# Kernel tuning notes

Measured on AMD Instinct MI355X. Metric: run time of the kernel, lower is better.

## Reference

```python
import jax, jax.numpy as jnp
import numpy as np
import math

D_MODEL = 1024
HEADS = 16
HEAD_DIM = D_MODEL // HEADS
FFN = 4096
B, S = 2, 2048


def _layer_norm(x, gamma, beta, eps=1e-5):
    mean = jnp.mean(x, axis=-1, keepdims=True)
    var = jnp.mean((x - mean) ** 2, axis=-1, keepdims=True)
    return gamma * (x - mean) / jnp.sqrt(var + eps) + beta


def _sdpa(q, k, v, mask):
    # q,k,v: [B,H,S,dh]; mask: [S,S] additive, broadcasts over B,H
    scaled = jnp.einsum('bhqd,bhkd->bhqk', q, k) / math.sqrt(q.shape[-1])
    scaled = scaled + mask
    attn = jax.nn.softmax(scaled, axis=-1)
    return jnp.einsum('bhqk,bhkd->bhqd', attn, v)


def setup_inputs() -> dict:
    key = jax.random.key(0)
    ks = jax.random.split(key, 12)
    s = 0.02
    inp = {
        'x': jax.random.normal(ks[0], (B, S, D_MODEL), jnp.float32),
        'y': jax.random.normal(ks[1], (B, S, D_MODEL), jnp.float32),
        'self_attention_mask': jnp.zeros((S, S), jnp.float32),
        'cross_attention_mask': jnp.zeros((S, S), jnp.float32),
        # self-attention params
        'Wqkv': jax.random.normal(ks[2], (D_MODEL, 3 * D_MODEL), jnp.float32) * s,
        'bqkv': jnp.zeros((3 * D_MODEL,), jnp.float32),
        'Wo1': jax.random.normal(ks[3], (D_MODEL, D_MODEL), jnp.float32) * s,
        'bo1': jnp.zeros((D_MODEL,), jnp.float32),
        # cross-attention params
        'Wkv': jax.random.normal(ks[4], (D_MODEL, 2 * D_MODEL), jnp.float32) * s,
        'bkv': jnp.zeros((2 * D_MODEL,), jnp.float32),
        'Wq': jax.random.normal(ks[5], (D_MODEL, D_MODEL), jnp.float32) * s,
        'bq': jnp.zeros((D_MODEL,), jnp.float32),
        'Wo2': jax.random.normal(ks[6], (D_MODEL, D_MODEL), jnp.float32) * s,
        'bo2': jnp.zeros((D_MODEL,), jnp.float32),
        # layer norms
        'g1': jnp.ones((D_MODEL,), jnp.float32), 'b1': jnp.zeros((D_MODEL,), jnp.float32),
        'g2': jnp.ones((D_MODEL,), jnp.float32), 'b2': jnp.zeros((D_MODEL,), jnp.float32),
        'g3': jnp.ones((D_MODEL,), jnp.float32), 'b3': jnp.zeros((D_MODEL,), jnp.float32),
        # FFN
        'W1': jax.random.normal(ks[7], (D_MODEL, FFN), jnp.float32) * s,
        'bw1': jnp.zeros((FFN,), jnp.float32),
        'W2': jax.random.normal(ks[8], (FFN, D_MODEL), jnp.float32) * s,
        'bw2': jnp.zeros((D_MODEL,), jnp.float32),
    }
    return inp


def reference(x, y, self_attention_mask, cross_attention_mask,
              Wqkv, bqkv, Wo1, bo1, Wkv, bkv, Wq, bq, Wo2, bo2,
              g1, b1, g2, b2, g3, b3, W1, bw1, W2, bw2):
    b, s, d = y.shape

    # ---- masked self-attention on y ----
    qkv = (y @ Wqkv + bqkv).reshape(b, s, HEADS, 3 * HEAD_DIM).transpose(0, 2, 1, 3)
    q, k, v = jnp.split(qkv, 3, axis=-1)  # each [B,H,S,dh]
    vals = _sdpa(q, k, v, self_attention_mask)
    vals = vals.transpose(0, 2, 1, 3).reshape(b, s, d)
    attn_out = vals @ Wo1 + bo1
    # dropout is identity at inference
    y1 = _layer_norm(attn_out + y, g1, b1)

    # ---- cross attention: q from y1, k/v from x ----
    kv = (x @ Wkv + bkv).reshape(b, s, HEADS, 2 * HEAD_DIM).transpose(0, 2, 1, 3)
    k2, v2 = jnp.split(kv, 2, axis=-1)
    q2 = (y1 @ Wq + bq).reshape(b, s, HEADS, HEAD_DIM).transpose(0, 2, 1, 3)
    vals2 = _sdpa(q2, k2, v2, cross_attention_mask)
    vals2 = vals2.transpose(0, 2, 1, 3).reshape(b, s, d)
    cross_out = vals2 @ Wo2 + bo2
    y2 = _layer_norm(cross_out + y1, g2, b2)

    # ---- FFN ----
    h = jax.nn.relu(y2 @ W1 + bw1)
    ffn_out = h @ W2 + bw2
    y3 = _layer_norm(ffn_out + y2, g3, b3)
    return y3
```

## Files before the change

### kernel.cpp

```cpp
#include <hip/hip_runtime.h>
#include <hip/hip_bf16.h>

#define SEQ      2048
#define BATCH    2
#define DMODEL   1024
#define NHEADS   16
#define HDIM     64
#define FFN_DIM  4096
#define MROWS    (BATCH*SEQ)

typedef __attribute__((ext_vector_type(8))) short bf16x8;
typedef __attribute__((ext_vector_type(4))) float f32x4;

__device__ __forceinline__ unsigned short f2b(float f) {
    union { float f; unsigned int u; } v; v.f = f;
    unsigned int u = v.u;
    return (unsigned short)((u + 0x7FFFu + ((u >> 16) & 1u)) >> 16);
}
__device__ __forceinline__ float b2f(unsigned short h) {
    union { unsigned int u; float f; } v; v.u = ((unsigned int)h) << 16;
    return v.f;
}
__device__ __forceinline__ void gload_lds16(const void* g, void* l) {
    __builtin_amdgcn_global_load_lds((const __attribute__((address_space(1))) void*)g,
                                     (__attribute__((address_space(3))) void*)l, 16, 0, 0);
}

__global__ __launch_bounds__(256) void wtrans(const float* __restrict__ W,
                                              unsigned short* __restrict__ Wt,
                                              int K, int N) {
    __shared__ float t[32][33];
    const int n0 = blockIdx.x * 32, k0 = blockIdx.y * 32;
    const int tx = threadIdx.x, ty = threadIdx.y;
#pragma unroll
    for (int i = 0; i < 4; i++)
        t[ty + i * 8][tx] = W[(size_t)(k0 + ty + i * 8) * N + n0 + tx];
    __syncthreads();
#pragma unroll
    for (int i = 0; i < 4; i++) {
        const int n = ty + i * 8;
        Wt[(size_t)(n0 + n) * K + k0 + tx] = f2b(t[tx][n]);
    }
}

__global__ __launch_bounds__(256) void tobf16(const float* __restrict__ in,
                                              unsigned short* __restrict__ out, int n) {
    const int i = (blockIdx.x * 256 + threadIdx.x) * 8;
    if (i >= n) return;
    float4 a = *(const float4*)(in + i);
    float4 b = *(const float4*)(in + i + 4);
    unsigned short r[8] = {f2b(a.x), f2b(a.y), f2b(a.z), f2b(a.w),
                           f2b(b.x), f2b(b.y), f2b(b.z), f2b(b.w)};
    *(uint4*)(out + i) = *(const uint4*)r;
}

template <int RELU, int WF32, int WB16>
__global__ __launch_bounds__(256) void gemm_bt(const unsigned short* __restrict__ A,
                                               const unsigned short* __restrict__ Bt,
                                               const float* __restrict__ bias,
                                               float* __restrict__ Cf,
                                               unsigned short* __restrict__ Cb,
                                               int M, int N, int K) {
    __shared__ __align__(16) unsigned short As[128 * 32];
    __shared__ __align__(16) unsigned short Bs[128 * 32];
    const int tid  = threadIdx.x;
    const int lane = tid & 63;
    const int w    = tid >> 6;
    const int m0   = blockIdx.y << 7;
    const int n0   = blockIdx.x << 7;
    const int wr   = (w >> 1) << 6;
    const int wc   = (w & 1) << 6;
    const int srow = lane >> 2;
    const int scol = (lane & 3) << 3;

    f32x4 acc[4][4];
#pragma unroll
    for (int mi = 0; mi < 4; mi++)
#pragma unroll
        for (int ni = 0; ni < 4; ni++) acc[mi][ni] = (f32x4){0.f, 0.f, 0.f, 0.f};

    for (int k0 = 0; k0 < K; k0 += 32) {
#pragma unroll
        for (int t = 0; t < 2; t++) {
            const int rg  = w * 2 + t;
            const int row = (rg << 4) + srow;
            gload_lds16(A  + (size_t)(m0 + row) * K + k0 + scol, (char*)As + (rg << 10));
            gload_lds16(Bt + (size_t)(n0 + row) * K + k0 + scol, (char*)Bs + (rg << 10));
        }
        __syncthreads();
        const int fr = lane & 15;
        const int fk = (lane >> 4) << 3;
        bf16x8 af[4], bfr[4];
#pragma unroll
        for (int i = 0; i < 4; i++) {
            af[i]  = *(const bf16x8*)(As + (wr + (i << 4) + fr) * 32 + fk);
            bfr[i] = *(const bf16x8*)(Bs + (wc + (i << 4) + fr) * 32 + fk);
        }
#pragma unroll
        for (int mi = 0; mi < 4; mi++)
#pragma unroll
            for (int ni = 0; ni < 4; ni++)
                acc[mi][ni] = __builtin_amdgcn_mfma_f32_16x16x32_bf16(af[mi], bfr[ni], acc[mi][ni], 0, 0, 0);
        __syncthreads();
    }

    const int fr = lane & 15;
    const int fq = lane >> 4;
#pragma unroll
    for (int mi = 0; mi < 4; mi++) {
#pragma unroll
        for (int ni = 0; ni < 4; ni++) {
            const int col = n0 + wc + (ni << 4) + fr;
            const float bv = bias[col];
#pragma unroll
            for (int i = 0; i < 4; i++) {
                const int row = m0 + wr + (mi << 4) + (fq << 2) + i;
                float v = acc[mi][ni][i] + bv;
                if (RELU) v = fmaxf(v, 0.f);
                if (WF32) Cf[(size_t)row * N + col] = v;
                if (WB16) Cb[(size_t)row * N + col] = f2b(v);
            }
        }
    }
}

template <int WB16>
__global__ __launch_bounds__(256) void resid_ln(const float* __restrict__ xin,
                                                const float* __restrict__ res,
                                                const float* __restrict__ g,
                                                const float* __restrict__ b,
                                                float* __restrict__ outf,
                                                unsigned short* __restrict__ outb) {
    const int row = blockIdx.x;
    const int tid = threadIdx.x;
    const size_t base = (size_t)row * 1024 + tid * 4;
    float4 xv = *(const float4*)(xin + base);
    float4 rv = *(const float4*)(res + base);
    const float v0 = xv.x + rv.x, v1 = xv.y + rv.y, v2 = xv.z + rv.z, v3 = xv.w + rv.w;
    float s  = v0 + v1 + v2 + v3;
    float sq = v0 * v0 + v1 * v1 + v2 * v2 + v3 * v3;
#pragma unroll
    for (int off = 32; off; off >>= 1) { s += __shfl_xor(s, off); sq += __shfl_xor(sq, off); }
    __shared__ float red[8];
    if ((tid & 63) == 0) { red[tid >> 6] = s; red[4 + (tid >> 6)] = sq; }
    __syncthreads();
    s  = red[0] + red[1] + red[2] + red[3];
    sq = red[4] + red[5] + red[6] + red[7];
    const float mean = s * (1.0f / 1024.0f);
    const float var  = sq * (1.0f / 1024.0f) - mean * mean;
    const float inv  = rsqrtf(var + 1e-5f);
    const int col = tid * 4;
    float4 gv = *(const float4*)(g + col);
    float4 bv = *(const float4*)(b + col);
    const float o0 = (v0 - mean) * inv * gv.x + bv.x;
    const float o1 = (v1 - mean) * inv * gv.y + bv.y;
    const float o2 = (v2 - mean) * inv * gv.z + bv.z;
    const float o3 = (v3 - mean) * inv * gv.w + bv.w;
    float4 ov = {o0, o1, o2, o3};
    *(float4*)(outf + base) = ov;
    if (WB16) {
        uint2 u;
        u.x = (unsigned int)f2b(o0) | ((unsigned int)f2b(o1) << 16);
        u.y = (unsigned int)f2b(o2) | ((unsigned int)f2b(o3) << 16);
        *(uint2*)(outb + base) = u;
    }
}

__global__ __launch_bounds__(256) void attn_mfma(
    const unsigned short* __restrict__ Qb, int q_rs, int q_ho,
    const unsigned short* __restrict__ Kb, int k_rs, int k_ho,
    const unsigned short* __restrict__ Vb, int v_rs, int v_ho,
    const float* __restrict__ mask,
    unsigned short* __restrict__ Ob, int o_rs, int o_ho) {
    __shared__ __align__(16) unsigned short Kls[64 * 64];
    __shared__ __align__(16) unsigned short Vraw[64 * 64];
    __shared__ __align__(16) unsigned short QVt[64 * 64];
    __shared__ __align__(16) unsigned short Pls[4][16 * 64];

    const int tid  = threadIdx.x;
    const int lane = tid & 63;
    const int w    = tid >> 6;
    const int g    = lane >> 4;
    const int q15  = lane & 15;
    const int swz  = (lane & 7) << 4;
    const int bh   = blockIdx.y;
    const int b    = bh >> 4, h = bh & 15;
    const int q0   = blockIdx.x << 6;
    const size_t rowbase = (size_t)b * SEQ;

    char* Kc = (char*)Kls;
    char* Vc = (char*)Vraw;
    char* Tc = (char*)QVt;
    char* Pc = (char*)(&Pls[w][0]);

    const int hq = h * q_ho, hk = h * k_ho, hv = h * v_ho;

    auto stage2 = [&](const unsigned short* base, int rs, int hoff, int row0, char* ldsb) {
#pragma unroll
        for (int bb = 0; bb < 2; bb++) {
            const int c = tid + (bb << 8);
            const int r = c >> 3, ci = c & 7;
            gload_lds16(base + (rowbase + row0 + r) * (size_t)rs + hoff + ((ci ^ (r & 7)) << 3),
                        ldsb + ((c >> 6) << 10));
        }
    };

    stage2(Qb, q_rs, hq, q0, Tc);
    stage2(Kb, k_rs, hk, 0, Kc);
    stage2(Vb, v_rs, hv, 0, Vc);

    float m_run = -3.0e38f, l_run = 0.f;
    f32x4 oacc[4];
#pragma unroll
    for (int fd = 0; fd < 4; fd++) oacc[fd] = (f32x4){0.f, 0.f, 0.f, 0.f};

    __syncthreads();
    bf16x8 qf[2];
#pragma unroll
    for (int s = 0; s < 2; s++)
        qf[s] = *(const bf16x8*)(Tc + (w * 16 + q15) * 128 + (((s << 6) + (g << 4)) ^ swz));
    __syncthreads();

    const float* mrow_ptr = mask + (size_t)(q0 + w * 16 + q15) * SEQ;

    for (int t = 0; t < 32; t++) {
        const int kv0 = t << 6;
#pragma unroll
        for (int bb = 0; bb < 2; bb++) {
            const int kvb = bb * 32 + w * 8;
            unsigned short t8[8];
#pragma unroll
            for (int m = 0; m < 8; m++)
                t8[m] = *(const unsigned short*)(Vc + (kvb + m) * 128 + ((2 * lane) ^ (m << 4)));
            *(uint4*)(Tc + lane * 128 + ((2 * kvb) ^ swz)) = *(const uint4*)t8;
        }
        f32x4 sacc[4];
#pragma unroll
        for (int f = 0; f < 4; f++) sacc[f] = (f32x4){0.f, 0.f, 0.f, 0.f};
#pragma unroll
        for (int s = 0; s < 2; s++)
#pragma unroll
            for (int f = 0; f < 4; f++) {
                bf16x8 kf = *(const bf16x8*)(Kc + (f * 16 + q15) * 128 + (((s << 6) + (g << 4)) ^ swz));
                sacc[f] = __builtin_amdgcn_mfma_f32_16x16x32_bf16(kf, qf[s], sacc[f], 0, 0, 0);
            }
        float p[4][4];
        float mt = -3.0e38f;
#pragma unroll
        for (int f = 0; f < 4; f++) {
            float4 mk = *(const float4*)(mrow_ptr + kv0 + f * 16 + g * 4);
            const float* mkp = (const float*)&mk;
#pragma unroll
            for (int r = 0; r < 4; r++) {
                const float v = sacc[f][r] * 0.125f + mkp[r];
                p[f][r] = v;
                mt = fmaxf(mt, v);
            }
        }
        mt = fmaxf(mt, __shfl_xor(mt, 16));
        mt = fmaxf(mt, __shfl_xor(mt, 32));
        const float mnew  = fmaxf(m_run, mt);
        const float alpha = __expf(m_run - mnew);
        m_run = mnew;
        float lsum = 0.f;
#pragma unroll
        for (int f = 0; f < 4; f++)
#pragma unroll
            for (int r = 0; r < 4; r++) {
                const float e = __expf(p[f][r] - mnew);
                p[f][r] = e;
                lsum += e;
            }
        lsum += __shfl_xor(lsum, 16);
        lsum += __shfl_xor(lsum, 32);
        l_run = l_run * alpha + lsum;
#pragma unroll
        for (int f = 0; f < 4; f++) {
            const unsigned int w0 = (unsigned int)f2b(p[f][0]) | ((unsigned int)f2b(p[f][1]) << 16);
            const unsigned int w1 = (unsigned int)f2b(p[f][2]) | ((unsigned int)f2b(p[f][3]) << 16);
            const int bbase = ((f << 5) + (g << 3)) ^ swz;
            *(unsigned int*)(Pc + q15 * 128 + bbase)     = w0;
            *(unsigned int*)(Pc + q15 * 128 + bbase + 4) = w1;
        }
        __syncthreads();
        if (t < 31) {
            stage2(Kb, k_rs, hk, kv0 + 64, Kc);
            stage2(Vb, v_rs, hv, kv0 + 64, Vc);
        }
        float ar[4];
#pragma unroll
        for (int r = 0; r < 4; r++) ar[r] = __shfl(alpha, (g << 4) + (g << 2) + r);
#pragma unroll
        for (int fd = 0; fd < 4; fd++)
#pragma unroll
            for (int r = 0; r < 4; r++) oacc[fd][r] *= ar[r];
#pragma unroll
        for (int s = 0; s < 2; s++) {
            const bf16x8 pf = *(const bf16x8*)(Pc + q15 * 128 + (((s << 6) + (g << 4)) ^ swz));
#pragma unroll
            for (int fd = 0; fd < 4; fd++) {
                const bf16x8 vf = *(const bf16x8*)(Tc + (fd * 16 + q15) * 128 + (((s << 6) + (g << 4)) ^ swz));
                oacc[fd] = __builtin_amdgcn_mfma_f32_16x16x32_bf16(pf, vf, oacc[fd], 0, 0, 0);
            }
        }
        __syncthreads();
    }

    const float rl = 1.0f / l_run;
    float invr[4];
#pragma unroll
    for (int r = 0; r < 4; r++) invr[r] = __shfl(rl, (g << 4) + (g << 2) + r);
    const size_t orow0 = rowbase + q0 + w * 16;
#pragma unroll
    for (int fd = 0; fd < 4; fd++)
#pragma unroll
        for (int r = 0; r < 4; r++) {
            const int qq = (g << 2) + r;
            Ob[(orow0 + qq) * (size_t)o_rs + h * o_ho + fd * 16 + q15] = f2b(oacc[fd][r] * invr[r]);
        }
}

extern "C" void kernel_launch(void* const* d_in, const int* in_sizes, int n_in,
                              void* d_out, int out_size, void* d_ws, size_t ws_size,
                              hipStream_t stream) {
    const float* x     = (const float*)d_in[0];
    const float* y     = (const float*)d_in[1];
    const float* mask1 = (const float*)d_in[2];
    const float* mask2 = (const float*)d_in[3];
    const float* Wqkv  = (const float*)d_in[4];
    const float* bqkv  = (const float*)d_in[5];
    const float* Wo1   = (const float*)d_in[6];
    const float* bo1   = (const float*)d_in[7];
    const float* Wkv   = (const float*)d_in[8];
    const float* bkv   = (const float*)d_in[9];
    const float* Wq    = (const float*)d_in[10];
    const float* bq    = (const float*)d_in[11];
    const float* Wo2   = (const float*)d_in[12];
    const float* bo2   = (const float*)d_in[13];
    const float* g1    = (const float*)d_in[14];
    const float* b1    = (const float*)d_in[15];
    const float* g2    = (const float*)d_in[16];
    const float* b2    = (const float*)d_in[17];
    const float* g3    = (const float*)d_in[18];
    const float* b3    = (const float*)d_in[19];
    const float* W1    = (const float*)d_in[20];
    const float* bw1   = (const float*)d_in[21];
    const float* W2    = (const float*)d_in[22];
    const float* bw2   = (const float*)d_in[23];

    char* ws = (char*)d_ws;
    const size_t o_WqkvT = 0;
    const size_t o_Wo1T  = o_WqkvT + 6291456;
    const size_t o_WkvT  = o_Wo1T  + 2097152;
    const size_t o_WqT   = o_WkvT  + 4194304;
    const size_t o_Wo2T  = o_WqT   + 2097152;
    const size_t o_W1T   = o_Wo2T  + 2097152;
    const size_t o_W2T   = o_W1T   + 8388608;
    const size_t o_xbf   = o_W2T   + 8388608;
    const size_t o_ybf   = o_xbf   + 8388608;
    const size_t o_qkv   = o_ybf   + 8388608;
    const size_t o_vals  = o_qkv   + 25165824;
    const size_t o_tmp   = o_vals  + 8388608;
    const size_t o_y1    = o_tmp   + 16777216;
    const size_t o_y1bf  = o_y1    + 16777216;
    const size_t o_y2    = o_y1bf  + 8388608;
    const size_t o_y2bf  = o_y2    + 16777216;
    const size_t o_kv    = o_qkv;
    const size_t o_q2    = o_qkv + 16777216;
    const size_t o_hbf   = o_xbf;

    unsigned short* pWqkvT = (unsigned short*)(ws + o_WqkvT);
    unsigned short* pWo1T  = (unsigned short*)(ws + o_Wo1T);
    unsigned short* pWkvT  = (unsigned short*)(ws + o_WkvT);
    unsigned short* pWqT   = (unsigned short*)(ws + o_WqT);
    unsigned short* pWo2T  = (unsigned short*)(ws + o_Wo2T);
    unsigned short* pW1T   = (unsigned short*)(ws + o_W1T);
    unsigned short* pW2T   = (unsigned short*)(ws + o_W2T);
    unsigned short* pxbf   = (unsigned short*)(ws + o_xbf);
    unsigned short* pybf   = (unsigned short*)(ws + o_ybf);
    unsigned short* pqkv   = (unsigned short*)(ws + o_qkv);
    unsigned short* pvals  = (unsigned short*)(ws + o_vals);
    float*          ptmp   = (float*)(ws + o_tmp);
    float*          py1    = (float*)(ws + o_y1);
    unsigned short* py1bf  = (unsigned short*)(ws + o_y1bf);
    float*          py2    = (float*)(ws + o_y2);
    unsigned short* py2bf  = (unsigned short*)(ws + o_y2bf);
    unsigned short* pkv    = (unsigned short*)(ws + o_kv);
    unsigned short* pq2    = (unsigned short*)(ws + o_q2);
    unsigned short* phbf   = (unsigned short*)(ws + o_hbf);

    const dim3 tb(32, 8);
    wtrans<<<dim3(3072 / 32, 1024 / 32), tb, 0, stream>>>(Wqkv, pWqkvT, 1024, 3072);
    wtrans<<<dim3(1024 / 32, 1024 / 32), tb, 0, stream>>>(Wo1,  pWo1T,  1024, 1024);
    wtrans<<<dim3(2048 / 32, 1024 / 32), tb, 0, stream>>>(Wkv,  pWkvT,  1024, 2048);
    wtrans<<<dim3(1024 / 32, 1024 / 32), tb, 0, stream>>>(Wq,   pWqT,   1024, 1024);
    wtrans<<<dim3(1024 / 32, 1024 / 32), tb, 0, stream>>>(Wo2,  pWo2T,  1024, 1024);
    wtrans<<<dim3(4096 / 32, 1024 / 32), tb, 0, stream>>>(W1,   pW1T,   1024, 4096);
    wtrans<<<dim3(1024 / 32, 4096 / 32), tb, 0, stream>>>(W2,   pW2T,   4096, 1024);
    tobf16<<<dim3(MROWS * DMODEL / 2048), dim3(256), 0, stream>>>(x, pxbf, MROWS * DMODEL);
    tobf16<<<dim3(MROWS * DMODEL / 2048), dim3(256), 0, stream>>>(y, pybf, MROWS * DMODEL);

    gemm_bt<0, 0, 1><<<dim3(3072 / 128, MROWS / 128), dim3(256), 0, stream>>>(
        pybf, pWqkvT, bqkv, nullptr, pqkv, MROWS, 3072, 1024);
    attn_mfma<<<dim3(SEQ / 64, BATCH * NHEADS), dim3(256), 0, stream>>>(
        pqkv, 3072, 192, pqkv + 64, 3072, 192, pqkv + 128, 3072, 192,
        mask1, pvals, 1024, 64);
    gemm_bt<0, 1, 0><<<dim3(1024 / 128, MROWS / 128), dim3(256), 0, stream>>>(
        pvals, pWo1T, bo1, ptmp, nullptr, MROWS, 1024, 1024);
    resid_ln<1><<<dim3(MROWS), dim3(256), 0, stream>>>(ptmp, y, g1, b1, py1, py1bf);

    gemm_bt<0, 0, 1><<<dim3(2048 / 128, MROWS / 128), dim3(256), 0, stream>>>(
        pxbf, pWkvT, bkv, nullptr, pkv, MROWS, 2048, 1024);
    gemm_bt<0, 0, 1><<<dim3(1024 / 128, MROWS / 128), dim3(256), 0, stream>>>(
        py1bf, pWqT, bq, nullptr, pq2, MROWS, 1024, 1024);
    attn_mfma<<<dim3(SEQ / 64, BATCH * NHEADS), dim3(256), 0, stream>>>(
        pq2, 1024, 64, pkv, 2048, 128, pkv + 64, 2048, 128,
        mask2, pvals, 1024, 64);
    gemm_bt<0, 1, 0><<<dim3(1024 / 128, MROWS / 128), dim3(256), 0, stream>>>(
        pvals, pWo2T, bo2, ptmp, nullptr, MROWS, 1024, 1024);
    resid_ln<1><<<dim3(MROWS), dim3(256), 0, stream>>>(ptmp, py1, g2, b2, py2, py2bf);

    gemm_bt<1, 0, 1><<<dim3(4096 / 128, MROWS / 128), dim3(256), 0, stream>>>(
        py2bf, pW1T, bw1, nullptr, phbf, MROWS, 4096, 1024);
    gemm_bt<0, 1, 0><<<dim3(1024 / 128, MROWS / 128), dim3(256), 0, stream>>>(
        phbf, pW2T, bw2, ptmp, nullptr, MROWS, 1024, 4096);
    resid_ln<0><<<dim3(MROWS), dim3(256), 0, stream>>>(ptmp, py2, g3, b3, (float*)d_out, nullptr);
}
```

Baseline: 712.5 us.

## Add 256x256-tile pipelined bf16 GEMM for the wide projection GEMMs

Adds a new 512-thread GEMM kernel with 256x256 output tiles, double-buffered LDS filled via global_load_lds in four quarter-tile stages, XOR-swizzled LDS layout, explicit vmcnt waits and setprio around MFMA bursts. It replaces the 128x128 kernel for the QKV, cross-attention KV and FFN-up GEMMs, aiming for more data reuse per tile and better overlap of loads with MFMA. The larger tiles mean fewer blocks (e.g. 192 for QKV, 128 for KV), which may underfill the 256 CUs. The hand-placed waitcnt counts also add correctness risk.

```diff
diff --git a/kernel.cpp b/kernel.cpp
--- a/kernel.cpp
+++ b/kernel.cpp
@@ -11,6 +11,9 @@
 
 typedef __attribute__((ext_vector_type(8))) short bf16x8;
 typedef __attribute__((ext_vector_type(4))) float f32x4;
+
+#define GFENCE() asm volatile("" ::: "memory")
+#define SBAR()   do { GFENCE(); __builtin_amdgcn_s_barrier(); GFENCE(); } while (0)
 
 __device__ __forceinline__ unsigned short f2b(float f) {
     union { float f; unsigned int u; } v; v.f = f;
@@ -122,6 +125,142 @@
             }
         }
     }
+}
+
+template <int RELU, int WF32, int WB16>
+__global__ __launch_bounds__(512, 2) void gemm256(const unsigned short* __restrict__ A,
+                                                  const unsigned short* __restrict__ Bt,
+                                                  const float* __restrict__ bias,
+                                                  float* __restrict__ Cf,
+                                                  unsigned short* __restrict__ Cb,
+                                                  int M, int N, int K) {
+    __shared__ __align__(16) unsigned short lds[2][2][256 * 64];
+    const int tid  = threadIdx.x;
+    const int lane = tid & 63;
+    const int w    = tid >> 6;
+    const int q15  = lane & 15;
+    const int g    = lane >> 4;
+    const int m0   = blockIdx.y << 8;
+    const int n0   = blockIdx.x << 8;
+    const int wr   = (w >> 2) << 7;
+    const int wc   = (w & 3) << 6;
+
+    f32x4 acc[8][4];
+#pragma unroll
+    for (int m = 0; m < 8; m++)
+#pragma unroll
+        for (int n = 0; n < 4; n++) acc[m][n] = (f32x4){0.f, 0.f, 0.f, 0.f};
+
+    const int NT = K >> 6;
+
+    auto stage = [&](int which, int buf, int h, int kt, const unsigned short* src, int base0) {
+        char* ldsb = (char*)&lds[buf][which][0];
+#pragma unroll
+        for (int j = 0; j < 2; j++) {
+            const int c    = (w << 7) + (j << 6) + lane;
+            const int r    = c >> 3, ci = c & 7;
+            const int trow = ((r >> 6) << 7) + (h << 6) + (r & 63);
+            const int r0   = (w << 4) + (j << 3);
+            const int tr0  = ((r0 >> 6) << 7) + (h << 6) + (r0 & 63);
+            gload_lds16(src + (size_t)(base0 + trow) * K + (kt << 6) + ((ci ^ (r & 7)) << 3),
+                        ldsb + tr0 * 128);
+        }
+    };
+    auto ldA = [&](int buf, int row, int kc) -> bf16x8 {
+        return *(const bf16x8*)((const char*)&lds[buf][0][0] + row * 128 + ((kc ^ (row & 7)) << 4));
+    };
+    auto ldB = [&](int buf, int row, int kc) -> bf16x8 {
+        return *(const bf16x8*)((const char*)&lds[buf][1][0] + row * 128 + ((kc ^ (row & 7)) << 4));
+    };
+
+    stage(1, 0, 0, 0, Bt, n0);
+    stage(1, 0, 1, 0, Bt, n0);
+    stage(0, 0, 0, 0, A, m0);
+    stage(0, 0, 1, 0, A, m0);
+
+    for (int t = 0; t < NT; ++t) {
+        const int buf = t & 1, nb = buf ^ 1;
+        const bool st = (t + 1 < NT);
+        bf16x8 bfr[4], af[4];
+
+        if (st) { stage(1, nb, 0, t + 1, Bt, n0);
+                  asm volatile("s_waitcnt vmcnt(4)" ::: "memory"); }
+        else    { asm volatile("s_waitcnt vmcnt(2)" ::: "memory"); }
+        SBAR();
+#pragma unroll
+        for (int n = 0; n < 4; n++) bfr[n] = ldB(buf, wc + n * 16 + q15, g);
+#pragma unroll
+        for (int m = 0; m < 4; m++) af[m]  = ldA(buf, wr + m * 16 + q15, g);
+        __builtin_amdgcn_s_setprio(1);
+#pragma unroll
+        for (int m = 0; m < 4; m++)
+#pragma unroll
+            for (int n = 0; n < 4; n++)
+                acc[m][n] = __builtin_amdgcn_mfma_f32_16x16x32_bf16(af[m], bfr[n], acc[m][n], 0, 0, 0);
+        __builtin_amdgcn_s_setprio(0);
+        SBAR();
+
+        if (st) { stage(1, nb, 1, t + 1, Bt, n0);
+                  asm volatile("s_waitcnt vmcnt(4)" ::: "memory"); }
+        else    { asm volatile("s_waitcnt vmcnt(0)" ::: "memory"); }
+        SBAR();
+#pragma unroll
+        for (int m = 0; m < 4; m++) af[m] = ldA(buf, wr + 64 + m * 16 + q15, g);
+        __builtin_amdgcn_s_setprio(1);
+#pragma unroll
+        for (int m = 0; m < 4; m++)
+#pragma unroll
+            for (int n = 0; n < 4; n++)
+                acc[4 + m][n] = __builtin_amdgcn_mfma_f32_16x16x32_bf16(af[m], bfr[n], acc[4 + m][n], 0, 0, 0);
+        __builtin_amdgcn_s_setprio(0);
+        SBAR();
+
+        if (st) stage(0, nb, 0, t + 1, A, m0);
+        SBAR();
+#pragma unroll
+        for (int n = 0; n < 4; n++) bfr[n] = ldB(buf, wc + n * 16 + q15, 4 + g);
+#pragma unroll
+        for (int m = 0; m < 4; m++) af[m]  = ldA(buf, wr + m * 16 + q15, 4 + g);
+        __builtin_amdgcn_s_setprio(1);
+#pragma unroll
+        for (int m = 0; m < 4; m++)
+#pragma unroll
+            for (int n = 0; n < 4; n++)
+                acc[m][n] = __builtin_amdgcn_mfma_f32_16x16x32_bf16(af[m], bfr[n], acc[m][n], 0, 0, 0);
+        __builtin_amdgcn_s_setprio(0);
+        SBAR();
+
+        if (st) stage(0, nb, 1, t + 1, A, m0);
+        SBAR();
+#pragma unroll
+        for (int m = 0; m < 4; m++) af[m] = ldA(buf, wr + 64 + m * 16 + q15, 4 + g);
+        __builtin_amdgcn_s_setprio(1);
+#pragma unroll
+        for (int m = 0; m < 4; m++)
+#pragma unroll
+            for (int n = 0; n < 4; n++)
+                acc[4 + m][n] = __builtin_amdgcn_mfma_f32_16x16x32_bf16(af[m], bfr[n], acc[4 + m][n], 0, 0, 0);
+        __builtin_amdgcn_s_setprio(0);
+        SBAR();
+    }
+
+#pragma unroll
+    for (int mh = 0; mh < 2; mh++)
+#pragma unroll
+        for (int mf = 0; mf < 4; mf++)
+#pragma unroll
+            for (int nf = 0; nf < 4; nf++) {
+                const int col = n0 + wc + nf * 16 + q15;
+                const float bv = bias[col];
+#pragma unroll
+                for (int i = 0; i < 4; i++) {
+                    const int row = m0 + wr + mh * 64 + mf * 16 + (g << 2) + i;
+                    float v = acc[mh * 4 + mf][nf][i] + bv;
+                    if (RELU) v = fmaxf(v, 0.f);
+                    if (WF32) Cf[(size_t)row * N + col] = v;
+                    if (WB16) Cb[(size_t)row * N + col] = f2b(v);
+                }
+            }
 }
 
 template <int WB16>
@@ -400,7 +539,7 @@
     tobf16<<<dim3(MROWS * DMODEL / 2048), dim3(256), 0, stream>>>(x, pxbf, MROWS * DMODEL);
     tobf16<<<dim3(MROWS * DMODEL / 2048), dim3(256), 0, stream>>>(y, pybf, MROWS * DMODEL);
 
-    gemm_bt<0, 0, 1><<<dim3(3072 / 128, MROWS / 128), dim3(256), 0, stream>>>(
+    gemm256<0, 0, 1><<<dim3(3072 / 256, MROWS / 256), dim3(512), 0, stream>>>(
         pybf, pWqkvT, bqkv, nullptr, pqkv, MROWS, 3072, 1024);
     attn_mfma<<<dim3(SEQ / 64, BATCH * NHEADS), dim3(256), 0, stream>>>(
         pqkv, 3072, 192, pqkv + 64, 3072, 192, pqkv + 128, 3072, 192,
@@ -409,7 +548,7 @@
         pvals, pWo1T, bo1, ptmp, nullptr, MROWS, 1024, 1024);
     resid_ln<1><<<dim3(MROWS), dim3(256), 0, stream>>>(ptmp, y, g1, b1, py1, py1bf);
 
-    gemm_bt<0, 0, 1><<<dim3(2048 / 128, MROWS / 128), dim3(256), 0, stream>>>(
+    gemm256<0, 0, 1><<<dim3(2048 / 256, MROWS / 256), dim3(512), 0, stream>>>(
         pxbf, pWkvT, bkv, nullptr, pkv, MROWS, 2048, 1024);
     gemm_bt<0, 0, 1><<<dim3(1024 / 128, MROWS / 128), dim3(256), 0, stream>>>(
         py1bf, pWqT, bq, nullptr, pq2, MROWS, 1024, 1024);
@@ -420,7 +559,7 @@
         pvals, pWo2T, bo2, ptmp, nullptr, MROWS, 1024, 1024);
     resid_ln<1><<<dim3(MROWS), dim3(256), 0, stream>>>(ptmp, py1, g2, b2, py2, py2bf);
 
-    gemm_bt<1, 0, 1><<<dim3(4096 / 128, MROWS / 128), dim3(256), 0, stream>>>(
+    gemm256<1, 0, 1><<<dim3(4096 / 256, MROWS / 256), dim3(512), 0, stream>>>(
         py2bf, pW1T, bw1, nullptr, phbf, MROWS, 4096, 1024);
     gemm_bt<0, 1, 0><<<dim3(1024 / 128, MROWS / 128), dim3(256), 0, stream>>>(
         phbf, pW2T, bw2, ptmp, nullptr, MROWS, 1024, 4096);
```

Result: no change. 704.2 us (-1.2%).
